# Optimization experiments

Measured on AMD Instinct MI355X. Metric: run time of the kernel, lower is better.

Reference implementation:

```python
import jax, jax.numpy as jnp
import numpy as np

N_NODES = 100000
N_EDGES = 3200000
IN_DIM, HID, N_LAB = 128, 64, 121


def setup_inputs() -> dict:
    key = jax.random.key(0)
    ks = jax.random.split(key, 8)
    x = jax.random.normal(ks[0], (N_NODES, IN_DIM), dtype=jnp.float32)
    edge_index = jax.random.randint(ks[1], (2, N_EDGES), 0, N_NODES, dtype=jnp.int64)
    W1 = jax.random.normal(ks[2], (IN_DIM, HID), dtype=jnp.float32) * (1.0 / np.sqrt(IN_DIM))
    b1 = jnp.zeros((HID,), dtype=jnp.float32)
    W2 = jax.random.normal(ks[3], (HID, HID), dtype=jnp.float32) * (1.0 / np.sqrt(HID))
    b2 = jnp.zeros((HID,), dtype=jnp.float32)
    Wout = jax.random.normal(ks[4], (HID, N_LAB), dtype=jnp.float32) * (1.0 / np.sqrt(HID))
    bout = jnp.zeros((N_LAB,), dtype=jnp.float32)
    return {"x": x, "edge_index": edge_index, "W1": W1, "b1": b1,
            "W2": W2, "b2": b2, "Wout": Wout, "bout": bout}


def _gcn_conv(x, W, b, src, dst, norm, n):
    # x' = D^{-1/2}(A+I)D^{-1/2} X W + b  (edges already include self-loops)
    xw = x @ W                                   # [N, out]
    msg = xw[src] * norm[:, None]                # [E+N, out] gather + scale
    agg = jax.ops.segment_sum(msg, dst, num_segments=n)  # scatter-add
    return agg + b


def reference(x, edge_index, W1, b1, W2, b2, Wout, bout):
    n = x.shape[0]
    loop = jnp.arange(n, dtype=edge_index.dtype)
    src = jnp.concatenate([edge_index[0], loop])
    dst = jnp.concatenate([edge_index[1], loop])
    # symmetric normalization (self-loops guarantee deg >= 1)
    deg = jax.ops.segment_sum(jnp.ones_like(dst, dtype=x.dtype), dst, num_segments=n)
    dinv = jax.lax.rsqrt(deg)
    norm = dinv[src] * dinv[dst]                 # [E+N]

    h = jax.nn.relu(_gcn_conv(x, W1, b1, src, dst, norm, n))
    # dropout p=0.5 is identity in eval mode (training=False)
    h = jax.nn.relu(_gcn_conv(h, W2, b2, src, dst, norm, n))
    logits = h @ Wout + bout                     # [N, num_labels]
    return logits
```

## Files before the change

### kernel.cpp

```cpp
#include <hip/hip_runtime.h>
#include <hip/hip_bf16.h>
#include <hip/hip_fp16.h>


#define IN_DIM 128
#define HID 64
#define N_LAB 121
#define NB_BLK 512

__global__ void scan1(const int* __restrict__ in, int* __restrict__ out,
                      int* __restrict__ bsums, int n) {
    __shared__ int s[256];
    int i = blockIdx.x * 256 + threadIdx.x;
    int v = (i < n) ? in[i] : 0;
    s[threadIdx.x] = v;
    __syncthreads();
    for (int off = 1; off < 256; off <<= 1) {
        int t = (threadIdx.x >= off) ? s[threadIdx.x - off] : 0;
        __syncthreads();
        s[threadIdx.x] += t;
        __syncthreads();
    }
    if (i < n) out[i] = s[threadIdx.x] - v;
    if (threadIdx.x == 255) bsums[blockIdx.x] = s[255];
}

__global__ __launch_bounds__(512) void bucket_count(const int* __restrict__ dst,
                                                    int* __restrict__ counts,
                                                    int nbuk, int chunk, int E) {
    __shared__ int c[512];
    for (int j = threadIdx.x; j < nbuk; j += 512) c[j] = 0;
    __syncthreads();
    int beg = blockIdx.x * chunk;
    int end = min(beg + chunk, E);
    int n = end - beg;
    if (n > 0) {
        const int2* p2 = (const int2*)(dst + beg);
        int nPair = n >> 1;
        for (int t = threadIdx.x; t < nPair; t += 512) {
            int2 d = p2[t];
            atomicAdd(&c[d.x >> 8], 1);
            atomicAdd(&c[d.y >> 8], 1);
        }
        if ((n & 1) && threadIdx.x == 0)
            atomicAdd(&c[dst[end - 1] >> 8], 1);
    }
    __syncthreads();
    for (int j = threadIdx.x; j < nbuk; j += 512)
        counts[j * NB_BLK + blockIdx.x] = c[j];
}

__device__ __forceinline__ void pair_scan_1024(const int* __restrict__ bsums,
                                               int* ps, int* bscan, int nb) {
    const int t = threadIdx.x;
    int pa = (2 * t     < nb) ? bsums[2 * t]     : 0;
    int pb = (2 * t + 1 < nb) ? bsums[2 * t + 1] : 0;
    ps[t] = pa + pb;
    __syncthreads();
    for (int off = 1; off < 512; off <<= 1) {
        int v = (t >= off) ? ps[t - off] : 0;
        __syncthreads();
        ps[t] += v;
        __syncthreads();
    }
    int excl = ps[t] - (pa + pb);
    bscan[2 * t]     = excl;
    bscan[2 * t + 1] = excl + pa;
    __syncthreads();
}

__global__ __launch_bounds__(512) void bucket_scatter(const int* __restrict__ src,
                                                      const int* __restrict__ dst,
                                                      const int* __restrict__ base,
                                                      const int* __restrict__ bsums,
                                                      int* __restrict__ bucketed,
                                                      int nbuk, int nbM,
                                                      int chunk, int E) {
    __shared__ int c[512];
    __shared__ int bs[512];
    __shared__ int ps[512];
    __shared__ int bscan[1024];
    pair_scan_1024(bsums, ps, bscan, nbM);
    for (int j = threadIdx.x; j < nbuk; j += 512) {
        c[j] = 0;
        int idx = j * NB_BLK + blockIdx.x;
        bs[j] = base[idx] + bscan[idx >> 8];
    }
    __syncthreads();
    int beg = blockIdx.x * chunk;
    int end = min(beg + chunk, E);
    int n = end - beg;
    if (n > 0) {
        const int2* d2 = (const int2*)(dst + beg);
        const int2* s2 = (const int2*)(src + beg);
        int nPair = n >> 1;
        for (int t = threadIdx.x; t < nPair; t += 512) {
            int2 d = d2[t];
            int2 s = s2[t];
            int b0 = d.x >> 8;
            int r0 = atomicAdd(&c[b0], 1);
            bucketed[bs[b0] + r0] = ((d.x & 255) << 17) | s.x;
            int b1 = d.y >> 8;
            int r1 = atomicAdd(&c[b1], 1);
            bucketed[bs[b1] + r1] = ((d.y & 255) << 17) | s.y;
        }
        if ((n & 1) && threadIdx.x == 0) {
            int d = dst[end - 1];
            int b = d >> 8;
            int r = atomicAdd(&c[b], 1);
            bucketed[bs[b] + r] = ((d & 255) << 17) | src[end - 1];
        }
    }
}

__global__ __launch_bounds__(512) void bucket_sort(const int* __restrict__ bucketed,
                                                   const int* __restrict__ base,
                                                   const int* __restrict__ bsums,
                                                   int* __restrict__ srcs,
                                                   int* __restrict__ row_ptr,
                                                   float* __restrict__ dinv,
                                                   int nbuk, int nbM, int N, int E) {
    __shared__ int h[512];
    __shared__ int cur[256];
    __shared__ int ps[512];
    __shared__ int bscan[1024];
    pair_scan_1024(bsums, ps, bscan, nbM);
    int b = blockIdx.x;
    int nodeBase = b << 8;
    int idx0 = b * NB_BLK;
    int s = base[idx0] + bscan[idx0 >> 8];
    int e;
    if (b == nbuk - 1) {
        e = E;
    } else {
        int idx1 = (b + 1) * NB_BLK;
        e = base[idx1] + bscan[idx1 >> 8];
    }
    h[threadIdx.x] = 0;
    __syncthreads();
    for (int i = s + threadIdx.x; i < e; i += 512)
        atomicAdd(&h[bucketed[i] >> 17], 1);
    __syncthreads();
    int v = h[threadIdx.x];
    for (int off = 1; off < 512; off <<= 1) {
        int t = (threadIdx.x >= off) ? h[threadIdx.x - off] : 0;
        __syncthreads();
        h[threadIdx.x] += t;
        __syncthreads();
    }
    if (threadIdx.x < 256) {
        int excl = h[threadIdx.x] - v;
        cur[threadIdx.x] = excl;
        int node = nodeBase + threadIdx.x;
        if (node < N) {
            row_ptr[node] = s + excl;
            dinv[node] = rsqrtf((float)v + 1.0f);
        }
    }
    if (b == nbuk - 1 && threadIdx.x == 0) row_ptr[N] = E;
    __syncthreads();
    for (int i = s + threadIdx.x; i < e; i += 512) {
        int p = bucketed[i];
        int d = p >> 17;
        int r = atomicAdd(&cur[d], 1);
        srcs[s + r] = (p & 0x1FFFF) << 7;
    }
}

template <int K, int N, int ROWS, typename OT>
__global__ __launch_bounds__(256) void gemm_kernel(
        const float* __restrict__ A, const float* __restrict__ B,
        const float* __restrict__ bias, const float* __restrict__ rowscale,
        OT* __restrict__ C, int M) {
    constexpr int NPAD = (N <= 64) ? 64 : 128;
    constexpr int CG = NPAD / 4;
    constexpr int RG = 256 / CG;
    constexpr int RPT = ROWS / RG;
    __shared__ float Bs[K * NPAD];

    for (int i = threadIdx.x; i < K * NPAD; i += 256) {
        int c = i & (NPAD - 1);
        int k = i / NPAD;
        Bs[i] = (c < N) ? B[k * N + c] : 0.f;
    }
    __syncthreads();

    const int cg = threadIdx.x % CG;
    const int rg = threadIdx.x / CG;
    const int row_base = blockIdx.x * ROWS;

    const float* Arow[RPT];
    #pragma unroll
    for (int j = 0; j < RPT; ++j) {
        int r = row_base + rg + RG * j;
        if (r > M - 1) r = M - 1;
        Arow[j] = A + (size_t)r * K;
    }

    float acc[RPT][4];
    #pragma unroll
    for (int j = 0; j < RPT; ++j) {
        acc[j][0] = 0.f; acc[j][1] = 0.f; acc[j][2] = 0.f; acc[j][3] = 0.f;
    }

    for (int k = 0; k < K; k += 4) {
        float4 Bq[4];
        #pragma unroll
        for (int kk = 0; kk < 4; ++kk)
            Bq[kk] = *(const float4*)&Bs[(k + kk) * NPAD + cg * 4];
        #pragma unroll
        for (int j = 0; j < RPT; ++j) {
            const float4 Aq = *(const float4*)(Arow[j] + k);
            #pragma unroll
            for (int c = 0; c < 4; ++c) {
                const float b0 = ((const float*)&Bq[0])[c];
                const float b1 = ((const float*)&Bq[1])[c];
                const float b2 = ((const float*)&Bq[2])[c];
                const float b3 = ((const float*)&Bq[3])[c];
                float a = acc[j][c];
                a = fmaf(Aq.x, b0, a);
                a = fmaf(Aq.y, b1, a);
                a = fmaf(Aq.z, b2, a);
                a = fmaf(Aq.w, b3, a);
                acc[j][c] = a;
            }
        }
    }

    float bv[4];
    #pragma unroll
    for (int c = 0; c < 4; ++c) {
        int col = cg * 4 + c;
        bv[c] = (bias && col < N) ? bias[col] : 0.f;
    }

    #pragma unroll
    for (int j = 0; j < RPT; ++j) {
        const int r = row_base + rg + RG * j;
        if (r >= M) continue;
        const float sc = rowscale ? rowscale[r] : 1.0f;
        float o[4];
        #pragma unroll
        for (int c = 0; c < 4; ++c) o[c] = fmaf(acc[j][c], sc, bv[c]);
        OT* Crow = C + (size_t)r * N;
        if constexpr (sizeof(OT) == 4 && (N % 4 == 0)) {
            *(float4*)&Crow[cg * 4] = make_float4(o[0], o[1], o[2], o[3]);
        } else if constexpr (sizeof(OT) == 2 && (N % 4 == 0)) {
            __half2* p = (__half2*)&Crow[cg * 4];
            p[0] = __floats2half2_rn(o[0], o[1]);
            p[1] = __floats2half2_rn(o[2], o[3]);
        } else {
            #pragma unroll
            for (int c = 0; c < 4; ++c) {
                int col = cg * 4 + c;
                if (col < N) Crow[col] = (OT)o[c];
            }
        }
    }
}

__global__ __launch_bounds__(256) void aggregate(
        const __half* __restrict__ feat2, const int* __restrict__ rp,
        const int* __restrict__ srcs, const float* __restrict__ dinv,
        const float* __restrict__ bias, float* __restrict__ out, int N) {
    const int wid = (int)((((size_t)blockIdx.x * 256) + threadIdx.x) >> 6);
    if (wid >= N) return;
    const int lane = threadIdx.x & 63;
    const int slot = lane >> 3;
    const int oct  = lane & 7;
    const char* fbB = (const char*)feat2 + oct * 16;

    float acc[8];
    #pragma unroll
    for (int i = 0; i < 8; ++i) acc[i] = 0.f;

    if (slot == 0) {
        const uint4 q = *(const uint4*)(fbB + ((size_t)wid << 7));
        const __half2* h = (const __half2*)&q;
        #pragma unroll
        for (int i = 0; i < 4; ++i) {
            const float2 f = __half22float2(h[i]);
            acc[2 * i]     += f.x;
            acc[2 * i + 1] += f.y;
        }
    }

    const int beg = rp[wid], end = rp[wid + 1];
    int idx = beg + slot;
    while (__any(idx < end)) {
        const bool p0 = idx < end;
        const bool p1 = (idx + 8) < end;
        const int i0 = p0 ? idx : beg;
        const int i1 = p1 ? (idx + 8) : beg;
        const int o0 = srcs[i0];
        const int o1 = srcs[i1];
        uint4 q0 = *(const uint4*)(fbB + o0);
        uint4 q1 = *(const uint4*)(fbB + o1);
        if (!p0) { q0.x = 0u; q0.y = 0u; q0.z = 0u; q0.w = 0u; }
        if (!p1) { q1.x = 0u; q1.y = 0u; q1.z = 0u; q1.w = 0u; }
        const __half2* h0 = (const __half2*)&q0;
        const __half2* h1 = (const __half2*)&q1;
        #pragma unroll
        for (int i = 0; i < 4; ++i) {
            const float2 f0 = __half22float2(h0[i]);
            const float2 f1 = __half22float2(h1[i]);
            acc[2 * i]     += f0.x + f1.x;
            acc[2 * i + 1] += f0.y + f1.y;
        }
        idx += 16;
    }

    #pragma unroll
    for (int m = 8; m <= 32; m <<= 1) {
        #pragma unroll
        for (int i = 0; i < 8; ++i)
            acc[i] += __shfl_xor(acc[i], m, 64);
    }

    if (slot == 0) {
        const float sc = dinv[wid];
        float o[8];
        #pragma unroll
        for (int i = 0; i < 8; ++i)
            o[i] = fmaxf(fmaf(acc[i], sc, bias[oct * 8 + i]), 0.f);
        float4* d4 = (float4*)(out + (((size_t)wid << 6) + oct * 8));
        d4[0] = make_float4(o[0], o[1], o[2], o[3]);
        d4[1] = make_float4(o[4], o[5], o[6], o[7]);
    }
}

extern "C" void kernel_launch(void* const* d_in, const int* in_sizes, int n_in,
                              void* d_out, int out_size, void* d_ws, size_t ws_size,
                              hipStream_t stream) {
    const float* x    = (const float*)d_in[0];
    const int*   ei   = (const int*)d_in[1];
    const float* W1   = (const float*)d_in[2];
    const float* b1   = (const float*)d_in[3];
    const float* W2   = (const float*)d_in[4];
    const float* b2   = (const float*)d_in[5];
    const float* Wout = (const float*)d_in[6];
    const float* bout = (const float*)d_in[7];
    float* out = (float*)d_out;

    const int N = in_sizes[0] / IN_DIM;
    const int E = in_sizes[1] / 2;
    const int* srcI = ei;
    const int* dstI = ei + E;

    const int nbuk = (N + 255) >> 8;
    const int M1 = nbuk * NB_BLK;
    const int chunk = (E + NB_BLK - 1) / NB_BLK;

    int*    row_ptr = (int*)d_ws;
    float*  dinv    = (float*)(row_ptr + (N + 1));
    int*    counts  = (int*)(dinv + N);
    int*    base    = counts + M1;
    int*    bsums   = base + M1;
    int*    srcs    = bsums + 1024;
    __half* feat2   = (__half*)(((uintptr_t)(srcs + E) + 15) & ~(uintptr_t)15);
    float*  hbuf    = (float*)(feat2 + (size_t)N * HID);
    int*    bucketed = (int*)feat2;

    const int nbM = (M1 + 255) / 256;
    const int gemmBlocks128 = (N + 127) / 128;
    const int gemmBlocks64  = (N + 63) / 64;
    const int aggBlocks = (int)(((size_t)N * HID + 255) / 256);

    bucket_count<<<NB_BLK, 512, 0, stream>>>(dstI, counts, nbuk, chunk, E);
    scan1<<<nbM, 256, 0, stream>>>(counts, base, bsums, M1);
    bucket_scatter<<<NB_BLK, 512, 0, stream>>>(srcI, dstI, base, bsums,
                                               bucketed, nbuk, nbM, chunk, E);
    bucket_sort<<<nbuk, 512, 0, stream>>>(bucketed, base, bsums, srcs, row_ptr,
                                          dinv, nbuk, nbM, N, E);

    gemm_kernel<IN_DIM, HID, 128, __half><<<gemmBlocks128, 256, 0, stream>>>(
        x, W1, nullptr, dinv, feat2, N);
    aggregate<<<aggBlocks, 256, 0, stream>>>(feat2, row_ptr, srcs, dinv, b1, hbuf, N);

    gemm_kernel<HID, HID, 128, __half><<<gemmBlocks128, 256, 0, stream>>>(
        hbuf, W2, nullptr, dinv, feat2, N);
    aggregate<<<aggBlocks, 256, 0, stream>>>(feat2, row_ptr, srcs, dinv, b2, hbuf, N);

    gemm_kernel<HID, N_LAB, 64, float><<<gemmBlocks64, 256, 0, stream>>>(
        hbuf, Wout, bout, nullptr, out, N);
}
```

Baseline: 484.4 us.

## Fuse following dense GEMMs into aggregation epilogue via wave shuffles

Each aggregation wave now applies bias and ReLU to its aggregated 64-wide row, then multiplies it by the next weight matrix (W2 or Wout) using lane shuffles and per-lane weight columns read from global memory. This removes two separate GEMM launches and the fp32 hidden-buffer round trip. In exchange, every wave does a 64xN matvec with uncoalesced-stride weight reads (cached) and 64 shuffles per output. The second layer writes fp32 logits directly with the output bias.

```diff
diff --git a/kernel.cpp b/kernel.cpp
--- a/kernel.cpp
+++ b/kernel.cpp
@@ -259,10 +259,13 @@
     }
 }
 
-__global__ __launch_bounds__(256) void aggregate(
+template <int NCOLS, typename OT>
+__global__ __launch_bounds__(256) void aggregate_fused(
         const __half* __restrict__ feat2, const int* __restrict__ rp,
         const int* __restrict__ srcs, const float* __restrict__ dinv,
-        const float* __restrict__ bias, float* __restrict__ out, int N) {
+        const float* __restrict__ bias, const float* __restrict__ W,
+        const float* __restrict__ bias2, OT* __restrict__ out, int N) {
+    constexpr bool SECOND = (NCOLS > 64);
     const int wid = (int)((((size_t)blockIdx.x * 256) + threadIdx.x) >> 6);
     if (wid >= N) return;
     const int lane = threadIdx.x & 63;
@@ -276,10 +279,10 @@
 
     if (slot == 0) {
         const uint4 q = *(const uint4*)(fbB + ((size_t)wid << 7));
-        const __half2* h = (const __half2*)&q;
+        const __half2* h2v = (const __half2*)&q;
         #pragma unroll
         for (int i = 0; i < 4; ++i) {
-            const float2 f = __half22float2(h[i]);
+            const float2 f = __half22float2(h2v[i]);
             acc[2 * i]     += f.x;
             acc[2 * i + 1] += f.y;
         }
@@ -317,15 +320,32 @@
             acc[i] += __shfl_xor(acc[i], m, 64);
     }
 
-    if (slot == 0) {
-        const float sc = dinv[wid];
-        float o[8];
-        #pragma unroll
-        for (int i = 0; i < 8; ++i)
-            o[i] = fmaxf(fmaf(acc[i], sc, bias[oct * 8 + i]), 0.f);
-        float4* d4 = (float4*)(out + (((size_t)wid << 6) + oct * 8));
-        d4[0] = make_float4(o[0], o[1], o[2], o[3]);
-        d4[1] = make_float4(o[4], o[5], o[6], o[7]);
+    const float sc = dinv[wid];
+    float h[8];
+    #pragma unroll
+    for (int i = 0; i < 8; ++i)
+        h[i] = fmaxf(fmaf(acc[i], sc, bias[oct * 8 + i]), 0.f);
+
+    const float* Wc1 = W + lane;
+    const float* Wc2 = W + (SECOND ? min(lane + 64, NCOLS - 1) : 0);
+    float a0 = 0.f, a1 = 0.f;
+    #pragma unroll
+    for (int s = 0; s < 8; ++s) {
+        #pragma unroll
+        for (int i = 0; i < 8; ++i) {
+            const float hv = __shfl(h[i], s, 64);
+            const int k = s * 8 + i;
+            a0 = fmaf(hv, Wc1[k * NCOLS], a0);
+            if constexpr (SECOND) a1 = fmaf(hv, Wc2[k * NCOLS], a1);
+        }
+    }
+
+    if constexpr (!SECOND) {
+        ((__half*)out)[((size_t)wid << 6) + lane] = __float2half(a0 * sc);
+    } else {
+        float* Crow = (float*)out + (size_t)wid * NCOLS;
+        Crow[lane] = a0 + bias2[lane];
+        if (lane < NCOLS - 64) Crow[64 + lane] = a1 + bias2[64 + lane];
     }
 }
 
@@ -357,13 +377,12 @@
     int*    base    = counts + M1;
     int*    bsums   = base + M1;
     int*    srcs    = bsums + 1024;
-    __half* feat2   = (__half*)(((uintptr_t)(srcs + E) + 15) & ~(uintptr_t)15);
-    float*  hbuf    = (float*)(feat2 + (size_t)N * HID);
-    int*    bucketed = (int*)feat2;
+    __half* feat2A  = (__half*)(((uintptr_t)(srcs + E) + 15) & ~(uintptr_t)15);
+    __half* feat2B  = feat2A + (size_t)N * HID;
+    int*    bucketed = (int*)feat2A;
 
     const int nbM = (M1 + 255) / 256;
     const int gemmBlocks128 = (N + 127) / 128;
-    const int gemmBlocks64  = (N + 63) / 64;
     const int aggBlocks = (int)(((size_t)N * HID + 255) / 256);
 
     bucket_count<<<NB_BLK, 512, 0, stream>>>(dstI, counts, nbuk, chunk, E);
@@ -374,13 +393,11 @@
                                           dinv, nbuk, nbM, N, E);
 
     gemm_kernel<IN_DIM, HID, 128, __half><<<gemmBlocks128, 256, 0, stream>>>(
-        x, W1, nullptr, dinv, feat2, N);
-    aggregate<<<aggBlocks, 256, 0, stream>>>(feat2, row_ptr, srcs, dinv, b1, hbuf, N);
-
-    gemm_kernel<HID, HID, 128, __half><<<gemmBlocks128, 256, 0, stream>>>(
-        hbuf, W2, nullptr, dinv, feat2, N);
-    aggregate<<<aggBlocks, 256, 0, stream>>>(feat2, row_ptr, srcs, dinv, b2, hbuf, N);
-
-    gemm_kernel<HID, N_LAB, 64, float><<<gemmBlocks64, 256, 0, stream>>>(
-        hbuf, Wout, bout, nullptr, out, N);
-}
+        x, W1, nullptr, dinv, feat2A, N);
+
+    aggregate_fused<64, __half><<<aggBlocks, 256, 0, stream>>>(
+        feat2A, row_ptr, srcs, dinv, b1, W2, nullptr, feat2B, N);
+
+    aggregate_fused<N_LAB, float><<<aggBlocks, 256, 0, stream>>>(
+        feat2B, row_ptr, srcs, dinv, b2, Wout, bout, out, N);
+}
```

After: 498.0 us. +2.8%, slower.
